# Kernel optimization log

Hardware: AMD Instinct MI355X
Metric: run time of the kernel (lower is better)

## Reference

```python
import jax, jax.numpy as jnp
import numpy as np
from jax.scipy.special import xlogy

B, N, F_IN, D, L = 32, 512, 20, 128, 5
NEG = -1e7


def setup_inputs() -> dict:
    key = jax.random.key(0)
    ks = jax.random.split(key, 24)
    s = lambda n: 1.0 / np.sqrt(n)
    inp = {}
    inp["fatoms"] = jax.random.normal(ks[0], (B, N, F_IN), jnp.float32)
    # normalized dense multi-relation adjacency (row sums ~1 for stability)
    inp["adj"] = jax.random.uniform(ks[1], (B, N, N, 3), jnp.float32) * (2.0 / N)
    inp["all_mask"] = jnp.ones((B, N, 1), jnp.float32)
    inp["current_mask"] = jnp.ones((B, N, 1), jnp.float32)
    inp["prob_mask"] = jnp.ones((B, N, 1), jnp.float32)
    inp["focus"] = jax.random.randint(ks[2], (B, 1), 0, N)
    inp["action_batch"] = jax.random.randint(ks[3], (B, 3), 0, 2)
    # embeddings (bias-free Linear(20, D))
    inp["W_emb"] = jax.random.normal(ks[4], (F_IN, D)) * s(F_IN)
    inp["W_cemb"] = jax.random.normal(ks[5], (F_IN, D)) * s(F_IN)
    # per-iteration, per-relation GCN weights [L,3,D,D] and biases [L,3,D]
    inp["actor_W"] = jax.random.normal(ks[6], (L, 3, D, D)) * s(D)
    inp["actor_b"] = jnp.zeros((L, 3, D), jnp.float32)
    inp["critic_W"] = jax.random.normal(ks[7], (L, 3, D, D)) * s(D)
    inp["critic_b"] = jnp.zeros((L, 3, D), jnp.float32)
    # end_selection_layer: Linear(2D,D)+ReLU+Linear(D,1,no bias)
    inp["We1"] = jax.random.normal(ks[8], (2 * D, D)) * s(2 * D)
    inp["be1"] = jnp.zeros((D,), jnp.float32)
    inp["We2"] = jax.random.normal(ks[9], (D, 1)) * s(D)
    # bond_selection_layer: Linear(2D,D)+ReLU+Linear(D,3,no bias)+Softmax
    inp["Wb1"] = jax.random.normal(ks[10], (2 * D, D)) * s(2 * D)
    inp["bb1"] = jnp.zeros((D,), jnp.float32)
    inp["Wb2"] = jax.random.normal(ks[11], (D, 3)) * s(D)
    # stop_selection_layer: Linear(D,D)+ReLU+Linear(D,2,no bias)+Softmax
    inp["Ws1"] = jax.random.normal(ks[12], (D, D)) * s(D)
    inp["bs1"] = jnp.zeros((D,), jnp.float32)
    inp["Ws2"] = jax.random.normal(ks[13], (D, 2)) * s(D)
    # qlayer: Linear(2D,D)+ReLU+Linear(D,1)
    inp["Wq1"] = jax.random.normal(ks[14], (2 * D, D)) * s(2 * D)
    inp["bq1"] = jnp.zeros((D,), jnp.float32)
    inp["Wq2"] = jax.random.normal(ks[15], (D, 1)) * s(D)
    inp["bq2"] = jnp.zeros((1,), jnp.float32)
    return inp


def _entropy(p):
    return -jnp.sum(xlogy(p, p), axis=-1)


def reference(fatoms, adj, all_mask, current_mask, prob_mask, focus, action_batch,
              W_emb, W_cemb, actor_W, actor_b, critic_W, critic_b,
              We1, be1, We2, Wb1, bb1, Wb2, Ws1, bs1, Ws2, Wq1, bq1, Wq2, bq2):
    def gcn_stack(x, Ws_all, bs_all):
        def step(h, wb):
            W, b = wb  # [3,D,D], [3,D]
            hw = jnp.einsum('bmd,rde->rbme', h, W) + b[:, None, None, :]
            msg = jax.nn.relu(jnp.einsum('bnmr,rbme->rbne', adj, hw))
            return jnp.sum(msg, axis=0) * all_mask, None
        h, _ = jax.lax.scan(step, x, (Ws_all, bs_all))
        return h

    # actor and critic feature updates
    x_a = gcn_stack(jax.nn.relu(fatoms @ W_emb), actor_W, actor_b)   # [B,N,D]
    x_c = gcn_stack(jax.nn.relu(fatoms @ W_cemb), critic_W, critic_b)

    # maxpool_sumpool + qlayer
    max_mask = jnp.where(current_mask == 1.0, 0.0, NEG)
    sum_pool = jnp.sum(x_c * current_mask, axis=1)                   # [B,D]
    max_pool = jnp.max(x_c + max_mask, axis=1)                       # [B,D]
    q_in = jnp.concatenate([sum_pool, max_pool], axis=-1)            # [B,2D]
    qvalue = jax.nn.relu(q_in @ Wq1 + bq1) @ Wq2 + bq2               # [B,1]

    pm = jnp.where(prob_mask == 1.0, 0.0, NEG)                       # [B,N,1]
    b, n, d = x_a.shape
    start = jnp.take_along_axis(x_a, jnp.broadcast_to(focus[:, :, None], (b, 1, d)), axis=1)  # [B,1,D]

    end_input = jnp.concatenate([jnp.broadcast_to(start, (b, n, d)), x_a], axis=-1)           # [B,N,2D]
    logits = jax.nn.relu(end_input @ We1 + be1) @ We2 + pm           # [B,N,1]
    end_probs = jax.nn.softmax(logits, axis=1)[..., 0]               # [B,N]

    end_idx = action_batch[:, 0:1]
    end_atom = jnp.take_along_axis(x_a, jnp.broadcast_to(end_idx[:, :, None], (b, 1, d)), axis=1)
    end_prob_new = jnp.take_along_axis(end_probs, end_idx, axis=1)   # [B,1]

    bond_in = jnp.concatenate([start, end_atom], axis=-1)[:, 0, :]   # [B,2D]
    bond_probs = jax.nn.softmax(jax.nn.relu(bond_in @ Wb1 + bb1) @ Wb2, axis=-1)  # [B,3]
    bond_prob_new = jnp.take_along_axis(bond_probs, action_batch[:, 1:2], axis=1)

    stop_probs = jax.nn.softmax(jax.nn.relu(start[:, 0, :] @ Ws1 + bs1) @ Ws2, axis=-1)  # [B,2]
    stop_prob_new = jnp.take_along_axis(stop_probs, action_batch[:, 2:3], axis=1)

    prob_batch_new = jnp.concatenate([end_prob_new, bond_prob_new, stop_prob_new], axis=-1)  # [B,3]
    entropy = _entropy(end_probs) + _entropy(bond_probs) + _entropy(stop_probs)             # [B]
    return prob_batch_new, entropy, qvalue
```

## Files before the change

kernel.cpp:

```cpp
#include <hip/hip_runtime.h>
#include <cstdint>
#include <cstddef>

typedef unsigned short u16;
typedef __bf16 bfx8 __attribute__((ext_vector_type(8)));
typedef float f32x4 __attribute__((ext_vector_type(4)));

#define NEGV -10000000.0f
constexpr int cB = 32, cN = 512, cD = 128, cF = 20, cL = 5;

__device__ __forceinline__ float bf2f(u16 h){ unsigned u = ((unsigned)h)<<16; return __builtin_bit_cast(float,u); }
__device__ __forceinline__ u16 f2bf(float f){ unsigned u = __builtin_bit_cast(unsigned,f); return (u16)((u + 0x7fffu + ((u>>16)&1u))>>16); }

constexpr int WOF_EMB  = 0;
constexpr int WOF_CEMB = 2560;
constexpr int WOF_AW   = 5120;
constexpr int WOF_CW   = 250880;
constexpr int WOF_WE1  = 496640;
constexpr int WOF_WE2  = 529408;
constexpr int WOF_WB1  = 529536;
constexpr int WOF_WB2  = 562304;
constexpr int WOF_WS1  = 562688;
constexpr int WOF_WS2  = 579072;
constexpr int WOF_WQ1  = 579328;
// ... 22 lines not shown
  constexpr int offs[13] = {WOF_EMB, WOF_CEMB, WOF_AW, WOF_CW, WOF_WE1, WOF_WE2,
                            WOF_WB1, WOF_WB2, WOF_WS1, WOF_WS2, WOF_WQ1, WOF_WQ2, WTOTAL};
  int a = 0;
  #pragma unroll
  for (int k = 1; k < 12; ++k) if (i >= offs[k]) a = k;
  int off = i - offs[a];
  const void* p = wp.p[a];
  Wc[i] = flag ? f2bf(((const float*)p)[off]) : ((const u16*)p)[off];
}

__global__ __launch_bounds__(256) void prep_w(const u16* __restrict__ Wc, u16* __restrict__ WT){
  __shared__ u16 sh[128*129];
  int blk = blockIdx.x;
  const u16* in;
  if (blk < 30){
    int s = blk/15; int lr = blk%15;
    in = Wc + (s ? WOF_CW : WOF_AW) + (size_t)lr*16384;
  } else {
    in = Wc + WOF_WE1 + 128*cD;
  }
  u16* out = WT + (size_t)blk*16384;
  int t = threadIdx.x;
  #pragma unroll 4
  for (int i=0;i<64;++i){ int idx=i*256+t; int d=idx>>7, e=idx&127; sh[e*129+d]=in[idx]; }
  __syncthreads();
  #pragma unroll 4
  for (int i=0;i<64;++i){ int idx=i*256+t; int e=idx>>7, d=idx&127; out[idx]=sh[e*129+d]; }
}

__global__ __launch_bounds__(128) void emb(const float* __restrict__ fatoms, const u16* __restrict__ Wc, u16* __restrict__ h0){
  int row = blockIdx.x;
  int s = row >> 14; int bn = row & 16383;
  __shared__ float fa[cF];
  int t = threadIdx.x;
  if (t < cF) fa[t] = fatoms[(size_t)bn*cF + t];
  __syncthreads();
  const u16* W = Wc + (s ? WOF_CEMB : WOF_EMB);
  float acc = 0.f;
  #pragma unroll
  for (int f=0; f<cF; ++f) acc += fa[f]*bf2f(W[f*cD + t]);
  h0[((size_t)s*cB*cN + bn)*cD + t] = f2bf(fmaxf(acc,0.f));
}

__device__ __forceinline__ void stage16k(const u16* gbase, int ldaB, int ktB, char* sm, int w, int l){
  #pragma unroll
  for (int i=0;i<4;++i){
    int c = (w<<2) + i;
    int row = (c<<3) + (l>>3);
    const char* src = (const char*)gbase + (size_t)row*ldaB + ktB + (((l&7)^(row&7))<<4);
    __builtin_amdgcn_global_load_lds((const __attribute__((address_space(1))) void*)src,
                                     (__attribute__((address_space(3))) void*)(sm + (c<<10)), 16, 0, 0);
  }
}
__device__ __forceinline__ void stage8k(const u16* gbase, int ldaB, int ktB, char* sm, int w, int l){
  #pragma unroll
  for (int i=0;i<2;++i){
    int c = (w<<1) + i;
    int row = (c<<3) + (l>>3);
    const char* src = (const char*)gbase + (size_t)row*ldaB + ktB + (((l&7)^(row&7))<<4);
    __builtin_amdgcn_global_load_lds((const __attribute__((address_space(1))) void*)src,
                                     (__attribute__((address_space(3))) void*)(sm + (c<<10)), 16, 0, 0);
  }
}
__device__ __forceinline__ bfx8 readfrag(const char* sm, int row, int kk, int l){
  int col = ((kk<<6) + ((l>>4)<<4)) ^ ((row&7)<<4);
  return *(const bfx8*)(sm + row*128 + col);
}
template<int MF,int NF>
__device__ __forceinline__ void mfma_tile(const char* A, const char* Bm, int ra, int rb, int l, f32x4 (&acc)[MF][NF]){
  #pragma unroll
  for (int kk=0; kk<2; ++kk){
    bfx8 af[MF], bv[NF];
    #pragma unroll
    for (int f=0; f<MF; ++f) af[f] = readfrag(A,  ra+(f<<4)+(l&15), kk, l);
    #pragma unroll
    for (int f=0; f<NF; ++f) bv[f] = readfrag(Bm, rb+(f<<4)+(l&15), kk, l);
    #pragma unroll
    for (int mf=0; mf<MF; ++mf)
      #pragma unroll
      for (int nf=0; nf<NF; ++nf)
        acc[mf][nf] = __builtin_amdgcn_mfma_f32_16x16x32_bf16(af[mf], bv[nf], acc[mf][nf], 0,0,0);
  }
}
__device__ __forceinline__ void flush16k(const char* P, char* gbase, int ldB, int colB, int t){
  #pragma unroll
  for (int j=0;j<4;++j){
    int p = j*4096 + t*16;
    int e = p>>7, col = p&127;
    int4 v = *(const int4*)(P + p);
    *(int4*)(gbase + (size_t)e*ldB + colB + col) = v;
  }
}

__global__ __launch_bounds__(256,2) void k1_hw(const u16* __restrict__ WT, const u16* __restrict__ h,
                                               const float* __restrict__ actor_b, const float* __restrict__ critic_b,
                                               u16* __restrict__ hwT, int layer){
  __shared__ __align__(16) char smA[16384];
  __shared__ __align__(16) char smB[16384];
  int blk = blockIdx.x;
  int nt = blk & 3; int srb = blk >> 2;
  int s = srb/96; int rb = srb%96; int r = rb>>5; int b = rb&31;
  int t = threadIdx.x, w = t>>6, l = t&63, wr = w>>1, wc = w&1;
  const u16* Abase = WT + (size_t)(s*15 + layer*3 + r)*16384;
  const u16* Bbase = h + ((size_t)s*cB*cN + (size_t)b*cN + (size_t)nt*128)*cD;
  f32x4 acc[4][4];
  #pragma unroll
  for (int i=0;i<4;++i){ acc[i][0]=f32x4{0,0,0,0}; acc[i][1]=f32x4{0,0,0,0}; acc[i][2]=f32x4{0,0,0,0}; acc[i][3]=f32x4{0,0,0,0}; }
  for (int kt=0; kt<2; ++kt){
    __syncthreads();
    stage16k(Abase, 256, kt*128, smA, w, l);
    stage16k(Bbase, 256, kt*128, smB, w, l);
    __syncthreads();
    mfma_tile<4,4>(smA, smB, wr<<6, wc<<6, l, acc);
  }
  const float* bias = (s ? critic_b : actor_b) + (layer*3 + r)*cD;
  __syncthreads();
  char* OPh = wc ? smB : smA;
  #pragma unroll
  for (int mf=0; mf<4; ++mf)
    #pragma unroll
    for (int nf=0; nf<4; ++nf)
      #pragma unroll
      for (int j=0; j<4; ++j){
        int e  = (wr<<6) + (mf<<4) + ((l>>4)<<2) + j;
        int mh = (nf<<4) + (l&15);
        *(u16*)(OPh + e*128 + mh*2) = f2bf(acc[mf][nf][j] + bias[e]);
      }
  __syncthreads();
  char* outB = (char*)(hwT + (size_t)((s*3+r)*cB + b)*cD*cN);
  flush16k(smA, outB, 1024, nt*256 + 0,   t);
  flush16k(smB, outB, 1024, nt*256 + 128, t);
}

template<int L0>
__global__ __launch_bounds__(256,2) void k2f(const float* __restrict__ adj, u16* __restrict__ adjT,
                                             const u16* __restrict__ hwT_in, u16* __restrict__ hwT_out,
                                             const float* __restrict__ all_mask, const u16* __restrict__ WT,
                                             const float* __restrict__ actor_b, const float* __restrict__ critic_b,
                                             u16* __restrict__ hfin, int layer){
  __shared__ __align__(16) char pool[73728];
  int blk = blockIdx.x;
  int xcd = blk & 7; int slot = blk >> 3;
  int b = (slot>>4)*8 + xcd;
  int rest = slot & 15; int s = rest>>3; int mt = rest&7;
  int t = threadIdx.x, w = t>>6, l = t&63, wr = w>>1, wc = w&1;
  const u16* hwB = hwT_in + (size_t)(s*3*cB + b)*cD*cN;
  const size_t hwRs = (size_t)cB*cD*cN;
  f32x4 sum[2][4];
  #pragma unroll
  for (int i=0;i<2;++i)
    #pragma unroll
    for (int j=0;j<4;++j) sum[i][j]=f32x4{0,0,0,0};

  if constexpr (L0){
    f32x4 a3[3][2][4];
    #pragma unroll
    for (int r=0;r<3;++r)
      #pragma unroll
      for (int i=0;i<2;++i)
        #pragma unroll
        for (int j=0;j<4;++j) a3[r][i][j]=f32x4{0,0,0,0};
    const int nl  = t>>2;
    const int m8  = (t&3)*2;
    const float* asrc = adj + ((size_t)(b*cN + mt*64 + nl)*cN + m8*8)*3;
    float4 v[12];
    #pragma unroll
    for (int q=0;q<12;++q) v[q] = ((const float4*)asrc)[q];
    for (int kt=0; kt<8; ++kt){
      __builtin_amdgcn_s_barrier();
      __builtin_amdgcn_sched_barrier(0);
      stage16k(hwB,        1024, kt*128, pool+24576, w, l);
      stage16k(hwB+hwRs,   1024, kt*128, pool+40960, w, l);
      stage16k(hwB+2*hwRs, 1024, kt*128, pool+57344, w, l);
      __builtin_amdgcn_sched_barrier(0);
      const float* vf = (const float*)v;
      __align__(16) u16 o[2][3][8];
      #pragma unroll
      for (int i=0;i<2;++i)
        #pragma unroll
        for (int r=0;r<3;++r)
          #pragma unroll
          for (int k=0;k<8;++k) o[i][r][k] = f2bf(vf[i*24 + k*3 + r]);
      #pragma unroll
      for (int i=0;i<2;++i){
        int m8i = m8 + i;
        #pragma unroll
        for (int r=0;r<3;++r)
          *(int4*)(pool + r*8192 + nl*128 + ((m8i*16) ^ ((nl&7)<<4))) = *(const int4*)&o[i][r][0];
      }
      if (kt < 7){
        const float* sp = asrc + (size_t)(kt+1)*64*3;
        #pragma unroll
        for (int q=0;q<12;++q) v[q] = ((const float4*)sp)[q];
      }
      __builtin_amdgcn_sched_barrier(0);
      if (kt < 7) asm volatile("s_waitcnt vmcnt(12)" ::: "memory");
      else        asm volatile("s_waitcnt vmcnt(0)"  ::: "memory");
      asm volatile("s_waitcnt lgkmcnt(0)" ::: "memory");
      __builtin_amdgcn_sched_barrier(0);
      __builtin_amdgcn_s_barrier();
      __builtin_amdgcn_sched_barrier(0);
      if (s == 0){
        #pragma unroll
        for (int r=0;r<3;++r){
          char* gb = (char*)adjT + (((size_t)(r*cB + b)*cN + (size_t)mt*64)*cN + (size_t)kt*64)*2;
          #pragma unroll
          for (int j=0;j<2;++j){
            int p = j*4096 + t*16;
            int n2 = p>>7, chunk = p&127;
            int4 val = *(const int4*)(pool + r*8192 + n2*128 + (chunk ^ ((n2&7)<<4)));
            *(int4*)(gb + (size_t)n2*1024 + chunk) = val;
          }
        }
      }
      #pragma unroll
      for (int r=0;r<3;++r)
        mfma_tile<2,4>(pool + r*8192, pool + 24576 + r*16384, wr<<5, wc<<6, l, a3[r]);
    }
    #pragma unroll
    for (int r=0;r<3;++r)
      #pragma unroll
      for (int mf=0;mf<2;++mf)
        #pragma unroll
        for (int nf=0;nf<4;++nf)
          #pragma unroll
          for (int j=0;j<4;++j)
            sum[mf][nf][j] += fmaxf(a3[r][mf][nf][j], 0.f);
  } else {
    const u16* adjB = adjT + ((size_t)b*cN + (size_t)mt*64)*cN;
    const size_t adjRs = (size_t)cB*cN*cN;
    for (int r=0;r<3;++r){
      f32x4 acc[2][4];
      #pragma unroll
      for (int i=0;i<2;++i)
        #pragma unroll
        for (int j=0;j<4;++j) acc[i][j]=f32x4{0,0,0,0};
      for (int kt=0;kt<8;++kt){
        __syncthreads();
        stage8k (adjB + (size_t)r*adjRs, 1024, kt*128, pool, w, l);
        stage16k(hwB  + (size_t)r*hwRs,  1024, kt*128, pool+8192, w, l);
        __syncthreads();
        mfma_tile<2,4>(pool, pool+8192, wr<<5, wc<<6, l, acc);
      }
      #pragma unroll
      for (int mf=0;mf<2;++mf)
        #pragma unroll
        for (int nf=0;nf<4;++nf)
          #pragma unroll
          for (int j=0;j<4;++j)
            sum[mf][nf][j] += fmaxf(acc[mf][nf][j], 0.f);
    }
  }
  __syncthreads();
  char* hT0 = pool + (L0 ? 0 : 24576);
  char* hT1 = hT0 + 8192;
  char* OP  = pool + (L0 ? 57344 : 0);
  #pragma unroll
  for (int mf=0; mf<2; ++mf)
    #pragma unroll
    for (int nf=0; nf<4; ++nf)
      #pragma unroll
      for (int j=0; j<4; ++j){
        int nloc = (wr<<5) + (mf<<4) + ((l>>4)<<2) + j;
        int e    = (wc<<6) + (nf<<4) + (l&15);
        int n    = mt*64 + nloc;
        u16 hv = f2bf(sum[mf][nf][j] * all_mask[b*cN + n]);
        char* base = (e & 64) ? hT1 : hT0;
        *(u16*)(base + nloc*128 + (((e&63)*2) ^ ((nloc&7)<<4))) = hv;
      }
  if (layer == cL-1){
    __syncthreads();
    char* gdst = (char*)(hfin + ((size_t)(s*cB + b)*cN + (size_t)mt*64)*cD);
    #pragma unroll
    for (int j=0;j<4;++j){
      int p = j*4096 + t*16;
      int nloc = p>>8, ebyte = p&255;
      char* hbase = (ebyte & 128) ? hT1 : hT0;
      int chunk = ebyte & 127;
      int4 v2 = *(const int4*)(hbase + nloc*128 + (chunk ^ ((nloc&7)<<4)));
      *(int4*)(gdst + (size_t)nloc*256 + ebyte) = v2;
    }
    return;
  }
  char* W0 = pool + (L0 ? 24576 : 40960);
  char* W1 = W0 + 16384;
  for (int r=0; r<3; ++r){
    __syncthreads();
    const u16* Wbase = WT + (size_t)(s*15 + (layer+1)*3 + r)*16384;
    stage16k(Wbase, 256, 0,   W0, w, l);
    stage16k(Wbase, 256, 128, W1, w, l);
    __syncthreads();
    f32x4 acc2[4][2];
    #pragma unroll
    for (int i=0;i<4;++i){ acc2[i][0]=f32x4{0,0,0,0}; acc2[i][1]=f32x4{0,0,0,0}; }
    mfma_tile<4,2>(W0, hT0, wr<<6, wc<<5, l, acc2);
    mfma_tile<4,2>(W1, hT1, wr<<6, wc<<5, l, acc2);
    const float* bias = (s ? critic_b : actor_b) + ((layer+1)*3 + r)*cD;
    #pragma unroll
    for (int mf=0; mf<4; ++mf)
      #pragma unroll
      for (int nf=0; nf<2; ++nf)
        #pragma unroll
        for (int j=0; j<4; ++j){
          int e   = (wr<<6) + (mf<<4) + ((l>>4)<<2) + j;
          int m64 = (wc<<5) + (nf<<4) + (l&15);
          *(u16*)(OP + e*128 + m64*2) = f2bf(acc2[mf][nf][j] + bias[e]);
        }
    __syncthreads();
    char* outB = (char*)(hwT_out + (size_t)((s*3+r)*cB + b)*cD*cN);
    flush16k(OP, outB, 1024, mt*128, t);
  }
}

__global__ __launch_bounds__(256) void pool_part(const u16* __restrict__ xc, const float* __restrict__ cmask,
                                                 float* __restrict__ part){
  int blk = blockIdx.x;
  int b = blk >> 4, c = blk & 15;
  int t = threadIdx.x; int d = t & 127, nh = t >> 7;
  const u16* x = xc + ((size_t)b*cN + c*32 + nh*16)*cD;
  const float* cm = cmask + (size_t)b*cN + c*32 + nh*16;
  float sm = 0.f, mx = -3e38f;
  #pragma unroll
  for (int i=0;i<16;++i){
    float v = bf2f(x[(size_t)i*cD + d]);
    float m = cm[i];
    sm += v*m;
    mx = fmaxf(mx, v + (m==1.0f ? 0.f : NEGV));
  }
  __shared__ float s_sm[2][128], s_mx[2][128];
  s_sm[nh][d] = sm; s_mx[nh][d] = mx;
  __syncthreads();
  if (nh == 0){
    float* dst = part + ((size_t)b*16 + c)*256;
    dst[d]       = sm + s_sm[1][d];
    dst[128 + d] = fmaxf(mx, s_mx[1][d]);
  }
}

__global__ __launch_bounds__(256,2) void end_logits2(const u16* __restrict__ xa, const u16* __restrict__ WT,
                                                     const u16* __restrict__ Wc, const int* __restrict__ focus,
                                                     const float* __restrict__ be1,
                                                     const float* __restrict__ prob_mask, float* __restrict__ logits){
  __shared__ __align__(16) char smA[16384];
  __shared__ __align__(16) char smB[16384];
  __shared__ float s_start[128], sh_sc[128], sh_w2[128], rowsum[2][128];
  int blk = blockIdx.x;
  int nt = blk & 3, b = blk >> 2;
  int t = threadIdx.x, w = t>>6, l = t&63, wr = w>>1, wc = w&1;
  if (t < 128){
    s_start[t] = bf2f(xa[((size_t)b*cN + focus[b])*cD + t]);
    sh_w2[t]   = bf2f(Wc[WOF_WE2 + t]);
  }
  __syncthreads();
  if (t < 128){
    float a = be1[t];
    #pragma unroll 4
    for (int k=0;k<128;++k) a += s_start[k]*bf2f(Wc[WOF_WE1 + k*cD + t]);
    sh_sc[t] = a;
  }
  const u16* Abase = xa + ((size_t)b*cN + (size_t)nt*128)*cD;
  const u16* Bbase = WT + (size_t)30*16384;
  f32x4 acc[4][4];
  #pragma unroll
// ... 109 lines not shown
  float r4 = hs*bf2f(Wc[WOF_WS2 + t*2+1]);
  #pragma unroll
  for (int o=32;o>0;o>>=1){
    r0 += __shfl_xor(r0,o,64); r1 += __shfl_xor(r1,o,64); r2 += __shfl_xor(r2,o,64);
    r3 += __shfl_xor(r3,o,64); r4 += __shfl_xor(r4,o,64);
  }
  if ((t&63)==0){ int wid=t>>6; red5[0][wid]=r0; red5[1][wid]=r1; red5[2][wid]=r2; red5[3][wid]=r3; red5[4][wid]=r4; }
  __syncthreads();
  if (t==0){
    out[128 + b] = redq[0] + redq[1] + bq2[0];
    auto xlx = [](float p){ return p > 0.f ? p*logf(p) : 0.f; };
    float bl0=red5[0][0]+red5[0][1], bl1=red5[1][0]+red5[1][1], bl2=red5[2][0]+red5[2][1];
    float sl0=red5[3][0]+red5[3][1], sl1=red5[4][0]+red5[4][1];
    float m = fmaxf(fmaxf(bl0,bl1),bl2);
    float e0=expf(bl0-m), e1=expf(bl1-m), e2=expf(bl2-m); float S=e0+e1+e2;
    float p0=e0/S, p1=e1/S, p2=e2/S;
    float Hb = -(xlx(p0) + xlx(p1) + xlx(p2));
    int a1 = action[b*3+1];
    out[b*3+1] = (a1==0)?p0:((a1==1)?p1:p2);
    float ms = fmaxf(sl0,sl1);
    float f0=expf(sl0-ms), f1=expf(sl1-ms); float T=f0+f1;
    float q0=f0/T, q1=f1/T;
    float Hs = -(xlx(q0) + xlx(q1));
    int a2 = action[b*3+2];
    out[b*3+2] = (a2==0)?q0:q1;
    out[96+b] = HendSh + Hb + Hs;
  }
}

extern "C" void kernel_launch(void* const* d_in, const int* in_sizes, int n_in,
                              void* d_out, int out_size, void* d_ws, size_t ws_size,
                              hipStream_t stream){
  const float* fatoms      = (const float*)d_in[0];
  const float* adj         = (const float*)d_in[1];
  const float* all_mask    = (const float*)d_in[2];
  const float* current_mask= (const float*)d_in[3];
  const float* prob_mask   = (const float*)d_in[4];
  const int*   focus       = (const int*)d_in[5];
  const int*   action      = (const int*)d_in[6];
  const float* actor_b     = (const float*)d_in[10];
  const float* critic_b    = (const float*)d_in[12];
  const float* be1         = (const float*)d_in[14];
  const float* bb1         = (const float*)d_in[17];
  const float* bs1         = (const float*)d_in[20];
  const float* bq1         = (const float*)d_in[23];
  const float* bq2         = (const float*)d_in[25];

  char* ws = (char*)d_ws;
  size_t o = 0;
  u16* adjT = (u16*)(ws + o);  o += (size_t)3*cB*cN*cN*2;
  u16* WT   = (u16*)(ws + o);  o += (size_t)31*16384*2;
  u16* hbuf = (u16*)(ws + o);  o += (size_t)2*2*cB*cN*cD*2;
  u16* hwT0 = (u16*)(ws + o);  o += (size_t)2*3*cB*cD*cN*2;
  u16* hwT1 = (u16*)(ws + o);  o += (size_t)2*3*cB*cD*cN*2;
  u16* Wcan = (u16*)(ws + o);  o += (size_t)WTOTAL*2;
  float* part   = (float*)(ws + o); o += (size_t)cB*16*256*4;
  float* logits = (float*)(ws + o); o += (size_t)cB*cN*4;
  float* out = (float*)d_out;

  WPtrs wp;
  wp.p[0]=d_in[7];  wp.p[1]=d_in[8];  wp.p[2]=d_in[9];  wp.p[3]=d_in[11];
  wp.p[4]=d_in[13]; wp.p[5]=d_in[15]; wp.p[6]=d_in[16]; wp.p[7]=d_in[18];
  wp.p[8]=d_in[19]; wp.p[9]=d_in[21]; wp.p[10]=d_in[22]; wp.p[11]=d_in[24];

  canon_w<<<dim3((WTOTAL+255)/256), dim3(256), 0, stream>>>(wp, Wcan);
  prep_w<<<dim3(31), dim3(256), 0, stream>>>(Wcan, WT);
  emb<<<dim3(2*cB*cN), dim3(128), 0, stream>>>(fatoms, Wcan, hbuf);

  const size_t hstride = (size_t)2*cB*cN*cD;
  u16* hfin = hbuf + hstride;
  k1_hw<<<dim3(768), dim3(256), 0, stream>>>(WT, hbuf, actor_b, critic_b, hwT0, 0);
  k2f<1><<<dim3(512), dim3(256), 0, stream>>>(adj, adjT, hwT0, hwT1, all_mask, WT, actor_b, critic_b, hfin, 0);
  for (int l=1; l<cL; ++l){
    u16* win  = (l&1) ? hwT1 : hwT0;
    u16* wout = (l&1) ? hwT0 : hwT1;
    k2f<0><<<dim3(512), dim3(256), 0, stream>>>(adj, adjT, win, wout, all_mask, WT, actor_b, critic_b, hfin, l);
  }
  const u16* xa = hfin;
  const u16* xc = hfin + (size_t)cB*cN*cD;

  end_logits2<<<dim3(cB*4), dim3(256), 0, stream>>>(xa, WT, Wcan, focus, be1, prob_mask, logits);
  pool_part<<<dim3(cB*16), dim3(256), 0, stream>>>(xc, current_mask, part);
  heads_final<<<dim3(cB), dim3(128), 0, stream>>>(part, Wcan, bq1, bq2, logits, action, xa, focus, bb1, bs1, out);
}
```

Baseline: 251.0 us.

## Split later GCN layer kernel into smaller 32-row tiles with higher occupancy

```diff
diff --git a/kernel.cpp b/kernel.cpp
--- a/kernel.cpp
+++ b/kernel.cpp
@@ -98,15 +98,12 @@
                                      (__attribute__((address_space(3))) void*)(sm + (c<<10)), 16, 0, 0);
   }
 }
-__device__ __forceinline__ void stage8k(const u16* gbase, int ldaB, int ktB, char* sm, int w, int l){
-  #pragma unroll
-  for (int i=0;i<2;++i){
-    int c = (w<<1) + i;
-    int row = (c<<3) + (l>>3);
-    const char* src = (const char*)gbase + (size_t)row*ldaB + ktB + (((l&7)^(row&7))<<4);
-    __builtin_amdgcn_global_load_lds((const __attribute__((address_space(1))) void*)src,
-                                     (__attribute__((address_space(3))) void*)(sm + (c<<10)), 16, 0, 0);
-  }
+__device__ __forceinline__ void stage4k(const u16* gbase, int ldaB, int ktB, char* sm, int w, int l){
+  int c = w;
+  int row = (c<<3) + (l>>3);
+  const char* src = (const char*)gbase + (size_t)row*ldaB + ktB + (((l&7)^(row&7))<<4);
+  __builtin_amdgcn_global_load_lds((const __attribute__((address_space(1))) void*)src,
+                                   (__attribute__((address_space(3))) void*)(sm + (c<<10)), 16, 0, 0);
 }
 __device__ __forceinline__ bfx8 readfrag(const char* sm, int row, int kk, int l){
   int col = ((kk<<6) + ((l>>4)<<4)) ^ ((row&7)<<4);
@@ -133,6 +130,15 @@
   for (int j=0;j<4;++j){
     int p = j*4096 + t*16;
     int e = p>>7, col = p&127;
+    int4 v = *(const int4*)(P + p);
+    *(int4*)(gbase + (size_t)e*ldB + colB + col) = v;
+  }
+}
+__device__ __forceinline__ void flush8k(const char* P, char* gbase, int ldB, int colB, int t){
+  #pragma unroll
+  for (int j=0;j<2;++j){
+    int p = j*4096 + t*16;
+    int e = p>>6, col = p&63;
     int4 v = *(const int4*)(P + p);
     *(int4*)(gbase + (size_t)e*ldB + colB + col) = v;
   }
@@ -178,12 +184,10 @@
   flush16k(smB, outB, 1024, nt*256 + 128, t);
 }
 
-template<int L0>
-__global__ __launch_bounds__(256,2) void k2f(const float* __restrict__ adj, u16* __restrict__ adjT,
-                                             const u16* __restrict__ hwT_in, u16* __restrict__ hwT_out,
-                                             const float* __restrict__ all_mask, const u16* __restrict__ WT,
-                                             const float* __restrict__ actor_b, const float* __restrict__ critic_b,
-                                             u16* __restrict__ hfin, int layer){
+__global__ __launch_bounds__(256,2) void k2f_l0(const float* __restrict__ adj, u16* __restrict__ adjT,
+                                                const u16* __restrict__ hwT_in, u16* __restrict__ hwT_out,
+                                                const float* __restrict__ all_mask, const u16* __restrict__ WT,
+                                                const float* __restrict__ actor_b, const float* __restrict__ critic_b){
   __shared__ __align__(16) char pool[73728];
   int blk = blockIdx.x;
   int xcd = blk & 7; int slot = blk >> 3;
@@ -198,109 +202,83 @@
     #pragma unroll
     for (int j=0;j<4;++j) sum[i][j]=f32x4{0,0,0,0};
 
-  if constexpr (L0){
-    f32x4 a3[3][2][4];
-    #pragma unroll
-    for (int r=0;r<3;++r)
-      #pragma unroll
-      for (int i=0;i<2;++i)
+  f32x4 a3[3][2][4];
+  #pragma unroll
+  for (int r=0;r<3;++r)
+    #pragma unroll
+    for (int i=0;i<2;++i)
+      #pragma unroll
+      for (int j=0;j<4;++j) a3[r][i][j]=f32x4{0,0,0,0};
+  const int nl  = t>>2;
+  const int m8  = (t&3)*2;
+  const float* asrc = adj + ((size_t)(b*cN + mt*64 + nl)*cN + m8*8)*3;
+  float4 v[12];
+  #pragma unroll
+  for (int q=0;q<12;++q) v[q] = ((const float4*)asrc)[q];
+  for (int kt=0; kt<8; ++kt){
+    __builtin_amdgcn_s_barrier();
+    __builtin_amdgcn_sched_barrier(0);
+    stage16k(hwB,        1024, kt*128, pool+24576, w, l);
+    stage16k(hwB+hwRs,   1024, kt*128, pool+40960, w, l);
+    stage16k(hwB+2*hwRs, 1024, kt*128, pool+57344, w, l);
+    __builtin_amdgcn_sched_barrier(0);
+    const float* vf = (const float*)v;
+    __align__(16) u16 o[2][3][8];
+    #pragma unroll
+    for (int i=0;i<2;++i)
+      #pragma unroll
+      for (int r=0;r<3;++r)
         #pragma unroll
-        for (int j=0;j<4;++j) a3[r][i][j]=f32x4{0,0,0,0};
-    const int nl  = t>>2;
-    const int m8  = (t&3)*2;
-    const float* asrc = adj + ((size_t)(b*cN + mt*64 + nl)*cN + m8*8)*3;
-    float4 v[12];
-    #pragma unroll
-    for (int q=0;q<12;++q) v[q] = ((const float4*)asrc)[q];
-    for (int kt=0; kt<8; ++kt){
-      __builtin_amdgcn_s_barrier();
-      __builtin_amdgcn_sched_barrier(0);
-      stage16k(hwB,        1024, kt*128, pool+24576, w, l);
-      stage16k(hwB+hwRs,   1024, kt*128, pool+40960, w, l);
-      stage16k(hwB+2*hwRs, 1024, kt*128, pool+57344, w, l);
-      __builtin_amdgcn_sched_barrier(0);
-      const float* vf = (const float*)v;
-      __align__(16) u16 o[2][3][8];
-      #pragma unroll
-      for (int i=0;i<2;++i)
+        for (int k=0;k<8;++k) o[i][r][k] = f2bf(vf[i*24 + k*3 + r]);
+    #pragma unroll
+    for (int i=0;i<2;++i){
+      int m8i = m8 + i;
+      #pragma unroll
+      for (int r=0;r<3;++r)
+        *(int4*)(pool + r*8192 + nl*128 + ((m8i*16) ^ ((nl&7)<<4))) = *(const int4*)&o[i][r][0];
+    }
+    if (kt < 7){
+      const float* sp = asrc + (size_t)(kt+1)*64*3;
+      #pragma unroll
+      for (int q=0;q<12;++q) v[q] = ((const float4*)sp)[q];
+    }
+    __builtin_amdgcn_sched_barrier(0);
+    if (kt < 7) asm volatile("s_waitcnt vmcnt(12)" ::: "memory");
+    else        asm volatile("s_waitcnt vmcnt(0)"  ::: "memory");
+    asm volatile("s_waitcnt lgkmcnt(0)" ::: "memory");
+    __builtin_amdgcn_sched_barrier(0);
+    __builtin_amdgcn_s_barrier();
+    __builtin_amdgcn_sched_barrier(0);
+    if (s == 0){
+      #pragma unroll
+      for (int r=0;r<3;++r){
+        char* gb = (char*)adjT + (((size_t)(r*cB + b)*cN + (size_t)mt*64)*cN + (size_t)kt*64)*2;
         #pragma unroll
-        for (int r=0;r<3;++r)
-          #pragma unroll
-          for (int k=0;k<8;++k) o[i][r][k] = f2bf(vf[i*24 + k*3 + r]);
-      #pragma unroll
-      for (int i=0;i<2;++i){
-        int m8i = m8 + i;
-        #pragma unroll
-        for (int r=0;r<3;++r)
-          *(int4*)(pool + r*8192 + nl*128 + ((m8i*16) ^ ((nl&7)<<4))) = *(const int4*)&o[i][r][0];
-      }
-      if (kt < 7){
-        const float* sp = asrc + (size_t)(kt+1)*64*3;
-        #pragma unroll
-        for (int q=0;q<12;++q) v[q] = ((const float4*)sp)[q];
-      }
-      __builtin_amdgcn_sched_barrier(0);
-      if (kt < 7) asm volatile("s_waitcnt vmcnt(12)" ::: "memory");
-      else        asm volatile("s_waitcnt vmcnt(0)"  ::: "memory");
-      asm volatile("s_waitcnt lgkmcnt(0)" ::: "memory");
-      __builtin_amdgcn_sched_barrier(0);
-      __builtin_amdgcn_s_barrier();
-      __builtin_amdgcn_sched_barrier(0);
-      if (s == 0){
-        #pragma unroll
-        for (int r=0;r<3;++r){
-          char* gb = (char*)adjT + (((size_t)(r*cB + b)*cN + (size_t)mt*64)*cN + (size_t)kt*64)*2;
-          #pragma unroll
-          for (int j=0;j<2;++j){
-            int p = j*4096 + t*16;
-            int n2 = p>>7, chunk = p&127;
-            int4 val = *(const int4*)(pool + r*8192 + n2*128 + (chunk ^ ((n2&7)<<4)));
-            *(int4*)(gb + (size_t)n2*1024 + chunk) = val;
-          }
+        for (int j=0;j<2;++j){
+          int p = j*4096 + t*16;
+          int n2 = p>>7, chunk = p&127;
+          int4 val = *(const int4*)(pool + r*8192 + n2*128 + (chunk ^ ((n2&7)<<4)));
+          *(int4*)(gb + (size_t)n2*1024 + chunk) = val;
         }
       }
-      #pragma unroll
-      for (int r=0;r<3;++r)
-        mfma_tile<2,4>(pool + r*8192, pool + 24576 + r*16384, wr<<5, wc<<6, l, a3[r]);
     }
     #pragma unroll
     for (int r=0;r<3;++r)
-      #pragma unroll
-      for (int mf=0;mf<2;++mf)
+      mfma_tile<2,4>(pool + r*8192, pool + 24576 + r*16384, wr<<5, wc<<6, l, a3[r]);
+  }
+  #pragma unroll
+  for (int r=0;r<3;++r)
+    #pragma unroll
+    for (int mf=0;mf<2;++mf)
+      #pragma unroll
+      for (int nf=0;nf<4;++nf)
         #pragma unroll
-        for (int nf=0;nf<4;++nf)
-          #pragma unroll
-          for (int j=0;j<4;++j)
-            sum[mf][nf][j] += fmaxf(a3[r][mf][nf][j], 0.f);
-  } else {
-    const u16* adjB = adjT + ((size_t)b*cN + (size_t)mt*64)*cN;
-    const size_t adjRs = (size_t)cB*cN*cN;
-    for (int r=0;r<3;++r){
-      f32x4 acc[2][4];
-      #pragma unroll
-      for (int i=0;i<2;++i)
-        #pragma unroll
-        for (int j=0;j<4;++j) acc[i][j]=f32x4{0,0,0,0};
-      for (int kt=0;kt<8;++kt){
-        __syncthreads();
-        stage8k (adjB + (size_t)r*adjRs, 1024, kt*128, pool, w, l);
-        stage16k(hwB  + (size_t)r*hwRs,  1024, kt*128, pool+8192, w, l);
-        __syncthreads();
-        mfma_tile<2,4>(pool, pool+8192, wr<<5, wc<<6, l, acc);
-      }
-      #pragma unroll
-      for (int mf=0;mf<2;++mf)
-        #pragma unroll
-        for (int nf=0;nf<4;++nf)
-          #pragma unroll
-          for (int j=0;j<4;++j)
-            sum[mf][nf][j] += fmaxf(acc[mf][nf][j], 0.f);
-    }
-  }
-  __syncthreads();
-  char* hT0 = pool + (L0 ? 0 : 24576);
-  char* hT1 = hT0 + 8192;
-  char* OP  = pool + (L0 ? 57344 : 0);
+        for (int j=0;j<4;++j)
+          sum[mf][nf][j] += fmaxf(a3[r][mf][nf][j], 0.f);
+  __syncthreads();
+  char* hT0 = pool;
+  char* hT1 = pool + 8192;
+  char* OP  = pool + 57344;
   #pragma unroll
   for (int mf=0; mf<2; ++mf)
     #pragma unroll
@@ -314,25 +292,11 @@
         char* base = (e & 64) ? hT1 : hT0;
         *(u16*)(base + nloc*128 + (((e&63)*2) ^ ((nloc&7)<<4))) = hv;
       }
-  if (layer == cL-1){
-    __syncthreads();
-    char* gdst = (char*)(hfin + ((size_t)(s*cB + b)*cN + (size_t)mt*64)*cD);
-    #pragma unroll
-    for (int j=0;j<4;++j){
-      int p = j*4096 + t*16;
-      int nloc = p>>8, ebyte = p&255;
-      char* hbase = (ebyte & 128) ? hT1 : hT0;
-      int chunk = ebyte & 127;
-      int4 v2 = *(const int4*)(hbase + nloc*128 + (chunk ^ ((nloc&7)<<4)));
-      *(int4*)(gdst + (size_t)nloc*256 + ebyte) = v2;
-    }
-    return;
-  }
-  char* W0 = pool + (L0 ? 24576 : 40960);
+  char* W0 = pool + 24576;
   char* W1 = W0 + 16384;
   for (int r=0; r<3; ++r){
     __syncthreads();
-    const u16* Wbase = WT + (size_t)(s*15 + (layer+1)*3 + r)*16384;
+    const u16* Wbase = WT + (size_t)(s*15 + 1*3 + r)*16384;
     stage16k(Wbase, 256, 0,   W0, w, l);
     stage16k(Wbase, 256, 128, W1, w, l);
     __syncthreads();
@@ -341,7 +305,7 @@
     for (int i=0;i<4;++i){ acc2[i][0]=f32x4{0,0,0,0}; acc2[i][1]=f32x4{0,0,0,0}; }
     mfma_tile<4,2>(W0, hT0, wr<<6, wc<<5, l, acc2);
     mfma_tile<4,2>(W1, hT1, wr<<6, wc<<5, l, acc2);
-    const float* bias = (s ? critic_b : actor_b) + ((layer+1)*3 + r)*cD;
+    const float* bias = (s ? critic_b : actor_b) + (1*3 + r)*cD;
     #pragma unroll
     for (int mf=0; mf<4; ++mf)
       #pragma unroll
@@ -355,6 +319,98 @@
     __syncthreads();
     char* outB = (char*)(hwT_out + (size_t)((s*3+r)*cB + b)*cD*cN);
     flush16k(OP, outB, 1024, mt*128, t);
+  }
+}
+
+__global__ __launch_bounds__(256,4) void k2f_ln(const u16* __restrict__ adjT,
+                                                const u16* __restrict__ hwT_in, u16* __restrict__ hwT_out,
+                                                const float* __restrict__ all_mask, const u16* __restrict__ WT,
+                                                const float* __restrict__ actor_b, const float* __restrict__ critic_b,
+                                                u16* __restrict__ hfin, int layer){
+  __shared__ __align__(16) char pool[28672];
+  int blk = blockIdx.x;
+  int xcd = blk & 7; int slot = blk >> 3;
+  int b = (slot>>5)*8 + xcd;
+  int rest = slot & 31; int s = rest>>4; int mt = rest&15;
+  int t = threadIdx.x, w = t>>6, l = t&63, wr = w>>1, wc = w&1;
+  const u16* hwB = hwT_in + (size_t)(s*3*cB + b)*cD*cN;
+  const size_t hwRs = (size_t)cB*cD*cN;
+  const u16* adjB = adjT + ((size_t)b*cN + (size_t)mt*32)*cN;
+  const size_t adjRs = (size_t)cB*cN*cN;
+  f32x4 sum[1][4];
+  #pragma unroll
+  for (int j=0;j<4;++j) sum[0][j]=f32x4{0,0,0,0};
+  for (int r=0;r<3;++r){
+    f32x4 acc[1][4];
+    #pragma unroll
+    for (int j=0;j<4;++j) acc[0][j]=f32x4{0,0,0,0};
+    for (int kt=0;kt<8;++kt){
+      __syncthreads();
+      stage4k (adjB + (size_t)r*adjRs, 1024, kt*128, pool, w, l);
+      stage16k(hwB  + (size_t)r*hwRs,  1024, kt*128, pool+4096, w, l);
+      __syncthreads();
+      mfma_tile<1,4>(pool, pool+4096, wr<<4, wc<<6, l, acc);
+    }
+    #pragma unroll
+    for (int nf=0;nf<4;++nf)
+      #pragma unroll
+      for (int j=0;j<4;++j)
+        sum[0][nf][j] += fmaxf(acc[0][nf][j], 0.f);
+  }
+  __syncthreads();
+  char* hT0 = pool + 20480;
+  char* hT1 = pool + 24576;
+  #pragma unroll
+  for (int nf=0; nf<4; ++nf)
+    #pragma unroll
+    for (int j=0; j<4; ++j){
+      int nloc = (wr<<4) + ((l>>4)<<2) + j;
+      int e    = (wc<<6) + (nf<<4) + (l&15);
+      int n    = mt*32 + nloc;
+      u16 hv = f2bf(sum[0][nf][j] * all_mask[b*cN + n]);
+      char* base = (e & 64) ? hT1 : hT0;
+      *(u16*)(base + nloc*128 + (((e&63)*2) ^ ((nloc&7)<<4))) = hv;
+    }
+  if (layer == cL-1){
+    __syncthreads();
+    char* gdst = (char*)(hfin + ((size_t)(s*cB + b)*cN + (size_t)mt*32)*cD);
+    #pragma unroll
+    for (int j=0;j<2;++j){
+      int p = j*4096 + t*16;
+      int nloc = p>>8, ebyte = p&255;
+      char* hbase = (ebyte & 128) ? hT1 : hT0;
+      int chunk = ebyte & 127;
+      int4 v2 = *(const int4*)(hbase + nloc*128 + (chunk ^ ((nloc&7)<<4)));
+      *(int4*)(gdst + (size_t)nloc*256 + ebyte) = v2;
+    }
+    return;
+  }
+  for (int r=0; r<3; ++r){
+    __syncthreads();
+    const u16* Wbase = WT + (size_t)(s*15 + (layer+1)*3 + r)*16384;
+    stage16k(Wbase, 256, 0, pool, w, l);
+    __syncthreads();
+    f32x4 acc2[4][1];
+    #pragma unroll
+    for (int i=0;i<4;++i) acc2[i][0]=f32x4{0,0,0,0};
+    mfma_tile<4,1>(pool, hT0, wr<<6, wc<<4, l, acc2);
+    __syncthreads();
+    stage16k(Wbase, 256, 128, pool, w, l);
+    __syncthreads();
+    mfma_tile<4,1>(pool, hT1, wr<<6, wc<<4, l, acc2);
+    __syncthreads();
+    const float* bias = (s ? critic_b : actor_b) + ((layer+1)*3 + r)*cD;
+    #pragma unroll
+    for (int mf=0; mf<4; ++mf)
+      #pragma unroll
+      for (int j=0; j<4; ++j){
+        int e   = (wr<<6) + (mf<<4) + ((l>>4)<<2) + j;
+        int m32 = (wc<<4) + (l&15);
+        *(u16*)(pool + e*64 + m32*2) = f2bf(acc2[mf][0][j] + bias[e]);
+      }
+    __syncthreads();
+    char* outB = (char*)(hwT_out + (size_t)((s*3+r)*cB + b)*cD*cN);
+    flush8k(pool, outB, 1024, mt*64, t);
   }
 }
 
@@ -588,11 +644,11 @@
   const size_t hstride = (size_t)2*cB*cN*cD;
   u16* hfin = hbuf + hstride;
   k1_hw<<<dim3(768), dim3(256), 0, stream>>>(WT, hbuf, actor_b, critic_b, hwT0, 0);
-  k2f<1><<<dim3(512), dim3(256), 0, stream>>>(adj, adjT, hwT0, hwT1, all_mask, WT, actor_b, critic_b, hfin, 0);
+  k2f_l0<<<dim3(512), dim3(256), 0, stream>>>(adj, adjT, hwT0, hwT1, all_mask, WT, actor_b, critic_b);
   for (int l=1; l<cL; ++l){
     u16* win  = (l&1) ? hwT1 : hwT0;
     u16* wout = (l&1) ? hwT0 : hwT1;
-    k2f<0><<<dim3(512), dim3(256), 0, stream>>>(adj, adjT, win, wout, all_mask, WT, actor_b, critic_b, hfin, l);
+    k2f_ln<<<dim3(1024), dim3(256), 0, stream>>>(adjT, win, wout, all_mask, WT, actor_b, critic_b, hfin, l);
   }
   const u16* xa = hfin;
   const u16* xc = hfin + (size_t)cB*cN*cD;
```

Result: slower. 263.2 us (+4.9%).

## Reassociate GCN layers to compute (A·h)·W with row-sum bias correction

Applied to the files above, without the earlier changes.

```diff
diff --git a/kernel.cpp b/kernel.cpp
--- a/kernel.cpp
+++ b/kernel.cpp
@@ -178,12 +178,9 @@
   flush16k(smB, outB, 1024, nt*256 + 128, t);
 }
 
-template<int L0>
-__global__ __launch_bounds__(256,2) void k2f(const float* __restrict__ adj, u16* __restrict__ adjT,
-                                             const u16* __restrict__ hwT_in, u16* __restrict__ hwT_out,
-                                             const float* __restrict__ all_mask, const u16* __restrict__ WT,
-                                             const float* __restrict__ actor_b, const float* __restrict__ critic_b,
-                                             u16* __restrict__ hfin, int layer){
+__global__ __launch_bounds__(256,2) void k2f_l0(const float* __restrict__ adj, u16* __restrict__ adjT,
+                                                const u16* __restrict__ hwT_in, u16* __restrict__ h1T,
+                                                float* __restrict__ rs, const float* __restrict__ all_mask){
   __shared__ __align__(16) char pool[73728];
   int blk = blockIdx.x;
   int xcd = blk & 7; int slot = blk >> 3;
@@ -198,109 +195,93 @@
     #pragma unroll
     for (int j=0;j<4;++j) sum[i][j]=f32x4{0,0,0,0};
 
-  if constexpr (L0){
-    f32x4 a3[3][2][4];
-    #pragma unroll
-    for (int r=0;r<3;++r)
-      #pragma unroll
-      for (int i=0;i<2;++i)
+  f32x4 a3[3][2][4];
+  #pragma unroll
+  for (int r=0;r<3;++r)
+    #pragma unroll
+    for (int i=0;i<2;++i)
+      #pragma unroll
+      for (int j=0;j<4;++j) a3[r][i][j]=f32x4{0,0,0,0};
+  float rsr[3] = {0.f, 0.f, 0.f};
+  const int nl  = t>>2;
+  const int m8  = (t&3)*2;
+  const float* asrc = adj + ((size_t)(b*cN + mt*64 + nl)*cN + m8*8)*3;
+  float4 v[12];
+  #pragma unroll
+  for (int q=0;q<12;++q) v[q] = ((const float4*)asrc)[q];
+  for (int kt=0; kt<8; ++kt){
+    __builtin_amdgcn_s_barrier();
+    __builtin_amdgcn_sched_barrier(0);
+    stage16k(hwB,        1024, kt*128, pool+24576, w, l);
+    stage16k(hwB+hwRs,   1024, kt*128, pool+40960, w, l);
+    stage16k(hwB+2*hwRs, 1024, kt*128, pool+57344, w, l);
+    __builtin_amdgcn_sched_barrier(0);
+    const float* vf = (const float*)v;
+    __align__(16) u16 o[2][3][8];
+    #pragma unroll
+    for (int i=0;i<2;++i)
+      #pragma unroll
+      for (int r=0;r<3;++r)
         #pragma unroll
-        for (int j=0;j<4;++j) a3[r][i][j]=f32x4{0,0,0,0};
-    const int nl  = t>>2;
-    const int m8  = (t&3)*2;
-    const float* asrc = adj + ((size_t)(b*cN + mt*64 + nl)*cN + m8*8)*3;
-    float4 v[12];
-    #pragma unroll
-    for (int q=0;q<12;++q) v[q] = ((const float4*)asrc)[q];
-    for (int kt=0; kt<8; ++kt){
-      __builtin_amdgcn_s_barrier();
-      __builtin_amdgcn_sched_barrier(0);
-      stage16k(hwB,        1024, kt*128, pool+24576, w, l);
-      stage16k(hwB+hwRs,   1024, kt*128, pool+40960, w, l);
-      stage16k(hwB+2*hwRs, 1024, kt*128, pool+57344, w, l);
-      __builtin_amdgcn_sched_barrier(0);
-      const float* vf = (const float*)v;
-      __align__(16) u16 o[2][3][8];
-      #pragma unroll
-      for (int i=0;i<2;++i)
+        for (int k=0;k<8;++k){
+          float raw = vf[i*24 + k*3 + r];
+          o[i][r][k] = f2bf(raw);
+          rsr[r] += raw;
+        }
+    #pragma unroll
+    for (int i=0;i<2;++i){
+      int m8i = m8 + i;
+      #pragma unroll
+      for (int r=0;r<3;++r)
+        *(int4*)(pool + r*8192 + nl*128 + ((m8i*16) ^ ((nl&7)<<4))) = *(const int4*)&o[i][r][0];
+    }
+    if (kt < 7){
+      const float* sp = asrc + (size_t)(kt+1)*64*3;
+      #pragma unroll
+      for (int q=0;q<12;++q) v[q] = ((const float4*)sp)[q];
+    }
+    __builtin_amdgcn_sched_barrier(0);
+    if (kt < 7) asm volatile("s_waitcnt vmcnt(12)" ::: "memory");
+    else        asm volatile("s_waitcnt vmcnt(0)"  ::: "memory");
+    asm volatile("s_waitcnt lgkmcnt(0)" ::: "memory");
+    __builtin_amdgcn_sched_barrier(0);
+    __builtin_amdgcn_s_barrier();
+    __builtin_amdgcn_sched_barrier(0);
+    if (s == 0){
+      #pragma unroll
+      for (int r=0;r<3;++r){
+        char* gb = (char*)adjT + (((size_t)(r*cB + b)*cN + (size_t)mt*64)*cN + (size_t)kt*64)*2;
         #pragma unroll
-        for (int r=0;r<3;++r)
-          #pragma unroll
-          for (int k=0;k<8;++k) o[i][r][k] = f2bf(vf[i*24 + k*3 + r]);
-      #pragma unroll
-      for (int i=0;i<2;++i){
-        int m8i = m8 + i;
-        #pragma unroll
-        for (int r=0;r<3;++r)
-          *(int4*)(pool + r*8192 + nl*128 + ((m8i*16) ^ ((nl&7)<<4))) = *(const int4*)&o[i][r][0];
-      }
-      if (kt < 7){
-        const float* sp = asrc + (size_t)(kt+1)*64*3;
-        #pragma unroll
-        for (int q=0;q<12;++q) v[q] = ((const float4*)sp)[q];
-      }
-      __builtin_amdgcn_sched_barrier(0);
-      if (kt < 7) asm volatile("s_waitcnt vmcnt(12)" ::: "memory");
-      else        asm volatile("s_waitcnt vmcnt(0)"  ::: "memory");
-      asm volatile("s_waitcnt lgkmcnt(0)" ::: "memory");
-      __builtin_amdgcn_sched_barrier(0);
-      __builtin_amdgcn_s_barrier();
-      __builtin_amdgcn_sched_barrier(0);
-      if (s == 0){
-        #pragma unroll
-        for (int r=0;r<3;++r){
-          char* gb = (char*)adjT + (((size_t)(r*cB + b)*cN + (size_t)mt*64)*cN + (size_t)kt*64)*2;
-          #pragma unroll
-          for (int j=0;j<2;++j){
-            int p = j*4096 + t*16;
-            int n2 = p>>7, chunk = p&127;
-            int4 val = *(const int4*)(pool + r*8192 + n2*128 + (chunk ^ ((n2&7)<<4)));
-            *(int4*)(gb + (size_t)n2*1024 + chunk) = val;
-          }
+        for (int j=0;j<2;++j){
+          int p = j*4096 + t*16;
+          int n2 = p>>7, chunk = p&127;
+          int4 val = *(const int4*)(pool + r*8192 + n2*128 + (chunk ^ ((n2&7)<<4)));
+          *(int4*)(gb + (size_t)n2*1024 + chunk) = val;
         }
       }
-      #pragma unroll
-      for (int r=0;r<3;++r)
-        mfma_tile<2,4>(pool + r*8192, pool + 24576 + r*16384, wr<<5, wc<<6, l, a3[r]);
     }
     #pragma unroll
     for (int r=0;r<3;++r)
-      #pragma unroll
-      for (int mf=0;mf<2;++mf)
+      mfma_tile<2,4>(pool + r*8192, pool + 24576 + r*16384, wr<<5, wc<<6, l, a3[r]);
+  }
+  #pragma unroll
+  for (int r=0;r<3;++r)
+    #pragma unroll
+    for (int mf=0;mf<2;++mf)
+      #pragma unroll
+      for (int nf=0;nf<4;++nf)
         #pragma unroll
-        for (int nf=0;nf<4;++nf)
-          #pragma unroll
-          for (int j=0;j<4;++j)
-            sum[mf][nf][j] += fmaxf(a3[r][mf][nf][j], 0.f);
-  } else {
-    const u16* adjB = adjT + ((size_t)b*cN + (size_t)mt*64)*cN;
-    const size_t adjRs = (size_t)cB*cN*cN;
-    for (int r=0;r<3;++r){
-      f32x4 acc[2][4];
-      #pragma unroll
-      for (int i=0;i<2;++i)
-        #pragma unroll
-        for (int j=0;j<4;++j) acc[i][j]=f32x4{0,0,0,0};
-      for (int kt=0;kt<8;++kt){
-        __syncthreads();
-        stage8k (adjB + (size_t)r*adjRs, 1024, kt*128, pool, w, l);
-        stage16k(hwB  + (size_t)r*hwRs,  1024, kt*128, pool+8192, w, l);
-        __syncthreads();
-        mfma_tile<2,4>(pool, pool+8192, wr<<5, wc<<6, l, acc);
-      }
-      #pragma unroll
-      for (int mf=0;mf<2;++mf)
-        #pragma unroll
-        for (int nf=0;nf<4;++nf)
-          #pragma unroll
-          for (int j=0;j<4;++j)
-            sum[mf][nf][j] += fmaxf(acc[mf][nf][j], 0.f);
-    }
-  }
-  __syncthreads();
-  char* hT0 = pool + (L0 ? 0 : 24576);
-  char* hT1 = hT0 + 8192;
-  char* OP  = pool + (L0 ? 57344 : 0);
+        for (int j=0;j<4;++j)
+          sum[mf][nf][j] += fmaxf(a3[r][mf][nf][j], 0.f);
+  #pragma unroll
+  for (int r=0;r<3;++r){
+    rsr[r] += __shfl_xor(rsr[r], 1, 64);
+    rsr[r] += __shfl_xor(rsr[r], 2, 64);
+    if (s == 0 && (t&3) == 0) rs[((size_t)r*cB + b)*cN + mt*64 + nl] = rsr[r];
+  }
+  __syncthreads();
+  char* hT0 = pool;
+  char* hT1 = pool + 8192;
   #pragma unroll
   for (int mf=0; mf<2; ++mf)
     #pragma unroll
@@ -314,47 +295,140 @@
         char* base = (e & 64) ? hT1 : hT0;
         *(u16*)(base + nloc*128 + (((e&63)*2) ^ ((nloc&7)<<4))) = hv;
       }
+  __syncthreads();
+  char* gdst = (char*)(h1T + (size_t)(s*cB + b)*cD*cN);
+  #pragma unroll
+  for (int j=0;j<4;++j){
+    int p = j*4096 + t*16;
+    int d = p>>7; int nbyte = p&127; int nbase = nbyte>>1;
+    char* panel = (d & 64) ? hT1 : hT0;
+    int colb = (d & 63)*2;
+    __align__(16) u16 o2[8];
+    #pragma unroll
+    for (int k=0;k<8;++k){
+      int nloc = nbase + k;
+      o2[k] = *(const u16*)(panel + nloc*128 + (colb ^ ((nloc&7)<<4)));
+    }
+    *(int4*)(gdst + (size_t)d*1024 + mt*128 + nbyte) = *(const int4*)o2;
+  }
+}
+
+__global__ __launch_bounds__(256,2) void k2g(const u16* __restrict__ adjT,
+                                             const u16* __restrict__ hT_in, u16* __restrict__ hT_out,
+                                             const float* __restrict__ all_mask, const u16* __restrict__ WT,
+                                             const float* __restrict__ actor_b, const float* __restrict__ critic_b,
+                                             const float* __restrict__ rs, u16* __restrict__ hfin, int layer){
+  __shared__ __align__(16) char pool[57344];
+  int blk = blockIdx.x;
+  int xcd = blk & 7; int slot = blk >> 3;
+  int b = (slot>>4)*8 + xcd;
+  int rest = slot & 15; int s = rest>>3; int mt = rest&7;
+  int t = threadIdx.x, w = t>>6, l = t&63, wr = w>>1, wc = w&1;
+  const u16* adjB = adjT + ((size_t)b*cN + (size_t)mt*64)*cN;
+  const size_t adjRs_ = (size_t)cB*cN*cN;
+  const u16* hTb = hT_in + (size_t)(s*cB + b)*cD*cN;
+  char* A  = pool;
+  char* Bp = pool + 8192;
+  char* P0 = pool + 24576;
+  char* P1 = pool + 32768;
+  char* W0 = pool;
+  char* W1 = pool + 40960;
+  f32x4 sum[2][4];
+  #pragma unroll
+  for (int i=0;i<2;++i)
+    #pragma unroll
+    for (int j=0;j<4;++j) sum[i][j]=f32x4{0,0,0,0};
+  for (int r=0; r<3; ++r){
+    f32x4 acc[2][4];
+    #pragma unroll
+    for (int i=0;i<2;++i)
+      #pragma unroll
+      for (int j=0;j<4;++j) acc[i][j]=f32x4{0,0,0,0};
+    for (int kt=0; kt<8; ++kt){
+      __syncthreads();
+      stage8k (adjB + (size_t)r*adjRs_, 1024, kt*128, A, w, l);
+      stage16k(hTb,                     1024, kt*128, Bp, w, l);
+      __syncthreads();
+      mfma_tile<2,4>(A, Bp, wr<<5, wc<<6, l, acc);
+    }
+    #pragma unroll
+    for (int mf=0; mf<2; ++mf)
+      #pragma unroll
+      for (int nf=0; nf<4; ++nf)
+        #pragma unroll
+        for (int j=0; j<4; ++j){
+          int nloc = (wr<<5) + (mf<<4) + ((l>>4)<<2) + j;
+          int d    = (wc<<6) + (nf<<4) + (l&15);
+          char* panel = (d & 64) ? P1 : P0;
+          *(u16*)(panel + nloc*128 + (((d&63)*2) ^ ((nloc&7)<<4))) = f2bf(acc[mf][nf][j]);
+        }
+    __syncthreads();
+    const u16* Wbase = WT + (size_t)(s*15 + layer*3 + r)*16384;
+    stage16k(Wbase, 256, 0,   W0, w, l);
+    stage16k(Wbase, 256, 128, W1, w, l);
+    __syncthreads();
+    f32x4 acc2[2][4];
+    #pragma unroll
+    for (int i=0;i<2;++i)
+      #pragma unroll
+      for (int j=0;j<4;++j) acc2[i][j]=f32x4{0,0,0,0};
+    mfma_tile<2,4>(P0, W0, wr<<5, wc<<6, l, acc2);
+    mfma_tile<2,4>(P1, W1, wr<<5, wc<<6, l, acc2);
+    const float* bias = (s ? critic_b : actor_b) + (layer*3 + r)*cD;
+    const float* rsr  = rs + ((size_t)r*cB + b)*cN + (size_t)mt*64;
+    #pragma unroll
+    for (int mf=0; mf<2; ++mf)
+      #pragma unroll
+      for (int nf=0; nf<4; ++nf)
+        #pragma unroll
+        for (int j=0; j<4; ++j){
+          int nloc = (wr<<5) + (mf<<4) + ((l>>4)<<2) + j;
+          int e    = (wc<<6) + (nf<<4) + (l&15);
+          sum[mf][nf][j] += fmaxf(acc2[mf][nf][j] + rsr[nloc]*bias[e], 0.f);
+        }
+  }
+  __syncthreads();
+  #pragma unroll
+  for (int mf=0; mf<2; ++mf)
+    #pragma unroll
+    for (int nf=0; nf<4; ++nf)
+      #pragma unroll
+      for (int j=0; j<4; ++j){
+        int nloc = (wr<<5) + (mf<<4) + ((l>>4)<<2) + j;
+        int e    = (wc<<6) + (nf<<4) + (l&15);
+        int n    = mt*64 + nloc;
+        u16 hv = f2bf(sum[mf][nf][j] * all_mask[b*cN + n]);
+        char* panel = (e & 64) ? P1 : P0;
+        *(u16*)(panel + nloc*128 + (((e&63)*2) ^ ((nloc&7)<<4))) = hv;
+      }
+  __syncthreads();
   if (layer == cL-1){
-    __syncthreads();
     char* gdst = (char*)(hfin + ((size_t)(s*cB + b)*cN + (size_t)mt*64)*cD);
     #pragma unroll
     for (int j=0;j<4;++j){
       int p = j*4096 + t*16;
       int nloc = p>>8, ebyte = p&255;
-      char* hbase = (ebyte & 128) ? hT1 : hT0;
+      char* panel = (ebyte & 128) ? P1 : P0;
       int chunk = ebyte & 127;
-      int4 v2 = *(const int4*)(hbase + nloc*128 + (chunk ^ ((nloc&7)<<4)));
+      int4 v2 = *(const int4*)(panel + nloc*128 + (chunk ^ ((nloc&7)<<4)));
       *(int4*)(gdst + (size_t)nloc*256 + ebyte) = v2;
     }
-    return;
-  }
-  char* W0 = pool + (L0 ? 24576 : 40960);
-  char* W1 = W0 + 16384;
-  for (int r=0; r<3; ++r){
-    __syncthreads();
-    const u16* Wbase = WT + (size_t)(s*15 + (layer+1)*3 + r)*16384;
-    stage16k(Wbase, 256, 0,   W0, w, l);
-    stage16k(Wbase, 256, 128, W1, w, l);
-    __syncthreads();
-    f32x4 acc2[4][2];
-    #pragma unroll
-    for (int i=0;i<4;++i){ acc2[i][0]=f32x4{0,0,0,0}; acc2[i][1]=f32x4{0,0,0,0}; }
-    mfma_tile<4,2>(W0, hT0, wr<<6, wc<<5, l, acc2);
-    mfma_tile<4,2>(W1, hT1, wr<<6, wc<<5, l, acc2);
-    const float* bias = (s ? critic_b : actor_b) + ((layer+1)*3 + r)*cD;
-    #pragma unroll
-    for (int mf=0; mf<4; ++mf)
-      #pragma unroll
-      for (int nf=0; nf<2; ++nf)
-        #pragma unroll
-        for (int j=0; j<4; ++j){
-          int e   = (wr<<6) + (mf<<4) + ((l>>4)<<2) + j;
-          int m64 = (wc<<5) + (nf<<4) + (l&15);
-          *(u16*)(OP + e*128 + m64*2) = f2bf(acc2[mf][nf][j] + bias[e]);
-        }
-    __syncthreads();
-    char* outB = (char*)(hwT_out + (size_t)((s*3+r)*cB + b)*cD*cN);
-    flush16k(OP, outB, 1024, mt*128, t);
+  } else {
+    char* gdst = (char*)(hT_out + (size_t)(s*cB + b)*cD*cN);
+    #pragma unroll
+    for (int j=0;j<4;++j){
+      int p = j*4096 + t*16;
+      int d = p>>7; int nbyte = p&127; int nbase = nbyte>>1;
+      char* panel = (d & 64) ? P1 : P0;
+      int colb = (d & 63)*2;
+      __align__(16) u16 o2[8];
+      #pragma unroll
+      for (int k=0;k<8;++k){
+        int nloc = nbase + k;
+        o2[k] = *(const u16*)(panel + nloc*128 + (colb ^ ((nloc&7)<<4)));
+      }
+      *(int4*)(gdst + (size_t)d*1024 + mt*128 + nbyte) = *(const int4*)o2;
+    }
   }
 }
 
@@ -570,8 +644,10 @@
   u16* WT   = (u16*)(ws + o);  o += (size_t)31*16384*2;
   u16* hbuf = (u16*)(ws + o);  o += (size_t)2*2*cB*cN*cD*2;
   u16* hwT0 = (u16*)(ws + o);  o += (size_t)2*3*cB*cD*cN*2;
-  u16* hwT1 = (u16*)(ws + o);  o += (size_t)2*3*cB*cD*cN*2;
+  u16* hTa  = (u16*)(ws + o);  o += (size_t)2*cB*cD*cN*2;
+  u16* hTb  = (u16*)(ws + o);  o += (size_t)2*cB*cD*cN*2;
   u16* Wcan = (u16*)(ws + o);  o += (size_t)WTOTAL*2;
+  float* rs     = (float*)(ws + o); o += (size_t)3*cB*cN*4;
   float* part   = (float*)(ws + o); o += (size_t)cB*16*256*4;
   float* logits = (float*)(ws + o); o += (size_t)cB*cN*4;
   float* out = (float*)d_out;
@@ -588,11 +664,11 @@
   const size_t hstride = (size_t)2*cB*cN*cD;
   u16* hfin = hbuf + hstride;
   k1_hw<<<dim3(768), dim3(256), 0, stream>>>(WT, hbuf, actor_b, critic_b, hwT0, 0);
-  k2f<1><<<dim3(512), dim3(256), 0, stream>>>(adj, adjT, hwT0, hwT1, all_mask, WT, actor_b, critic_b, hfin, 0);
+  k2f_l0<<<dim3(512), dim3(256), 0, stream>>>(adj, adjT, hwT0, hTa, rs, all_mask);
   for (int l=1; l<cL; ++l){
-    u16* win  = (l&1) ? hwT1 : hwT0;
-    u16* wout = (l&1) ? hwT0 : hwT1;
-    k2f<0><<<dim3(512), dim3(256), 0, stream>>>(adj, adjT, win, wout, all_mask, WT, actor_b, critic_b, hfin, l);
+    u16* tin  = (l&1) ? hTa : hTb;
+    u16* tout = (l&1) ? hTb : hTa;
+    k2g<<<dim3(512), dim3(256), 0, stream>>>(adjT, tin, tout, all_mask, WT, actor_b, critic_b, rs, hfin, l);
   }
   const u16* xa = hfin;
   const u16* xc = hfin + (size_t)cB*cN*cD;
```

Measured after the change: 256.1 us. +2.1%, slower.
